# Kernel tuning notes

Measured on AMD Instinct MI355X. Metric: run time of the kernel, lower is better.

Reference implementation:

```python
import jax, jax.numpy as jnp
import numpy as np

HID = 1024
BATCH = 32
SRC = 2048

def setup_inputs() -> dict:
    key = jax.random.key(0)
    k1, k2, k3, k4, k5 = jax.random.split(key, 5)
    hidden = jax.random.normal(k1, (BATCH, HID), dtype=jnp.float32)
    encoder_outputs = jax.random.normal(k2, (BATCH, SRC, HID), dtype=jnp.float32)
    # nn.Linear(2H, H): weight [H, 2H], bias [H]
    lim = 1.0 / np.sqrt(2 * HID)
    attn_w = jax.random.uniform(k3, (HID, 2 * HID), dtype=jnp.float32, minval=-lim, maxval=lim)
    attn_b = jax.random.uniform(k4, (HID,), dtype=jnp.float32, minval=-lim, maxval=lim)
    v = jax.random.uniform(k5, (HID,), dtype=jnp.float32)  # torch.rand
    return {"hidden": hidden, "encoder_outputs": encoder_outputs,
            "attn_w": attn_w, "attn_b": attn_b, "v": v}

def reference(hidden, encoder_outputs, attn_w, attn_b, v):
    # Split the concat linear: cat([hidden, enc]) @ W^T == hidden @ Wh^T + enc @ We^T
    w_h = attn_w[:, :HID]          # [H, H] acts on repeated hidden
    w_e = attn_w[:, HID:]          # [H, H] acts on encoder outputs
    # energy: [B, S, H]
    energy = jnp.tanh(
        jnp.einsum('bh,oh->bo', hidden, w_h)[:, None, :]
        + jnp.einsum('bsh,oh->bso', encoder_outputs, w_e)
        + attn_b
    )
    scores = jnp.einsum('bso,o->bs', energy, v)  # [B, S]
    return jax.nn.softmax(scores, axis=1)
```

## Files before the change

### kernel.cpp

```cpp
#include <hip/hip_runtime.h>
#include <hip/hip_bf16.h>

#define HID   1024
#define NBATCH 32
#define SRC   2048
#define MROWS (NBATCH * SRC)

typedef _Float16 f16;
typedef f16  f16x8 __attribute__((ext_vector_type(8)));
typedef f16  f16x4 __attribute__((ext_vector_type(4)));
typedef float f32x4 __attribute__((ext_vector_type(4)));

__device__ __forceinline__ void gload_lds16(const void* g, void* l) {
  __builtin_amdgcn_global_load_lds(
      (const __attribute__((address_space(1))) void*)g,
      (__attribute__((address_space(3))) void*)l, 16, 0, 0);
}

__device__ __forceinline__ float fast_tanh(float x) {
  x = fminf(fmaxf(x, -15.f), 15.f);
  float e = __expf(2.f * x);
  return (e - 1.f) / (e + 1.f);
}

__global__ void convw_k(const float* __restrict__ attn_w, f16* __restrict__ Wf) {
  int idx = blockIdx.x * 256 + threadIdx.x;
  int j = idx * 4;
  int o = j >> 10, h = j & 1023;
  f32x4 d = *(const f32x4*)(attn_w + (size_t)o * 2048 + HID + h);
  f16x4 q = { (f16)d[0], (f16)d[1], (f16)d[2], (f16)d[3] };
  *(f16x4*)(Wf + (size_t)o * HID + h) = q;
}

__global__ void hvec_k(const float* __restrict__ hidden,
                       const float* __restrict__ attn_w,
                       const float* __restrict__ attn_b,
                       float* __restrict__ hvec) {
  int idx = blockIdx.x * 256 + threadIdx.x;
  int b = idx >> 10, o = idx & 1023;
  const float* wrow = attn_w + (size_t)o * 2048;
  const float* hrow = hidden + (size_t)b * HID;
  float acc = 0.f;
  for (int h = 0; h < HID; h += 4) {
    f32x4 wv = *(const f32x4*)(wrow + h);
    f32x4 hv = *(const f32x4*)(hrow + h);
    acc += wv[0]*hv[0] + wv[1]*hv[1] + wv[2]*hv[2] + wv[3]*hv[3];
  }
  hvec[idx] = acc + attn_b[o];
}

__global__ __launch_bounds__(256, 2) void gemm_fused(
    const float* __restrict__ A,
    const f16*  __restrict__ Wf,
    const float* __restrict__ hvec,
    const float* __restrict__ v,
    float* __restrict__ part)
{
  __shared__ __align__(16) f16 lA[128][32];
  __shared__ __align__(16) f16 lB[128][32];
  __shared__ float sc[128];

  int bid = blockIdx.x;
  int x = bid & 7;
  int j = bid >> 3;
  int m_idx = x * 64 + (j >> 3);
  int n_idx = j & 7;
  long row0 = (long)m_idx * 128;
  int  o0   = n_idx * 128;
  int  b    = (int)(row0 >> 11);

  int tid = threadIdx.x;
  int l = tid & 63, w = tid >> 6;
  int wr = w >> 1, wc = w & 1;
  int lr = l & 15, lg = l >> 4;

  f32x4 acc[4][4];
#pragma unroll
  for (int m = 0; m < 4; ++m)
#pragma unroll
    for (int n = 0; n < 4; ++n) acc[m][n] = (f32x4){0.f, 0.f, 0.f, 0.f};

  const float* Abase = A + row0 * 1024;

  for (int k0 = 0; k0 < 1024; k0 += 32) {
    __syncthreads();
#pragma unroll
    for (int i = 0; i < 2; ++i) {
      int rr = (i * 256 + tid) >> 2;
      const f16* src = Wf + (size_t)(o0 + rr) * HID + k0 + (tid & 3) * 8;
      char* ldsb = (char*)&lB[0][0] + i * 4096 + w * 1024;
      gload_lds16(src, ldsb);
    }
#pragma unroll
    for (int i = 0; i < 4; ++i) {
      int ja = i * 256 + tid;
      int arow = ja >> 3, ac4 = ja & 7;
      f32x4 d = *(const f32x4*)(Abase + (size_t)arow * 1024 + k0 + ac4 * 4);
      f16x4 q = { (f16)d[0], (f16)d[1], (f16)d[2], (f16)d[3] };
      *(f16x4*)&lA[arow][ac4 * 4] = q;
    }
    __syncthreads();
    f16x8 aF[4], bF[4];
#pragma unroll
    for (int m = 0; m < 4; ++m)
      aF[m] = *(const f16x8*)&lA[wr * 64 + m * 16 + lr][lg * 8];
#pragma unroll
    for (int n = 0; n < 4; ++n)
      bF[n] = *(const f16x8*)&lB[wc * 64 + n * 16 + lr][lg * 8];
#pragma unroll
    for (int m = 0; m < 4; ++m)
#pragma unroll
      for (int n = 0; n < 4; ++n)
        acc[m][n] = __builtin_amdgcn_mfma_f32_16x16x32_f16(aF[m], bF[n], acc[m][n], 0, 0, 0);
  }

  float hv[4], vv[4];
#pragma unroll
  for (int n = 0; n < 4; ++n) {
    int o = o0 + wc * 64 + n * 16 + lr;
    hv[n] = hvec[b * HID + o];
    vv[n] = v[o];
  }
  float myv[4][4];
#pragma unroll
  for (int m = 0; m < 4; ++m) {
#pragma unroll
    for (int r = 0; r < 4; ++r) {
      float s = 0.f;
#pragma unroll
      for (int n = 0; n < 4; ++n) {
        float e = fast_tanh(acc[m][n][r] + hv[n]);
        s += e * vv[n];
      }
      s += __shfl_xor(s, 1);
      s += __shfl_xor(s, 2);
      s += __shfl_xor(s, 4);
      s += __shfl_xor(s, 8);
      myv[m][r] = s;
    }
  }
  if (wc == 0 && lr == 0) {
#pragma unroll
    for (int m = 0; m < 4; ++m)
#pragma unroll
      for (int r = 0; r < 4; ++r)
        sc[wr * 64 + m * 16 + lg * 4 + r] = myv[m][r];
  }
  __syncthreads();
  if (wc == 1 && lr == 0) {
#pragma unroll
    for (int m = 0; m < 4; ++m)
#pragma unroll
      for (int r = 0; r < 4; ++r)
        sc[wr * 64 + m * 16 + lg * 4 + r] += myv[m][r];
  }
  __syncthreads();
  if (tid < 128)
    part[(size_t)n_idx * MROWS + row0 + tid] = sc[tid];
}

__global__ void softmax_k(const float* __restrict__ part, float* __restrict__ out) {
  int b = blockIdx.x;
  __shared__ float srow[SRC];
  __shared__ float red[8];
  int tid = threadIdx.x;

  float lmax = -1e30f;
  for (int i = tid; i < SRC; i += 256) {
    float s = 0.f;
#pragma unroll
    for (int t = 0; t < 8; ++t)
      s += part[(size_t)t * MROWS + (size_t)b * SRC + i];
    srow[i] = s;
    lmax = fmaxf(lmax, s);
  }
#pragma unroll
  for (int off = 32; off >= 1; off >>= 1)
    lmax = fmaxf(lmax, __shfl_xor(lmax, off));
  if ((tid & 63) == 0) red[tid >> 6] = lmax;
  __syncthreads();
  float bmax = fmaxf(fmaxf(red[0], red[1]), fmaxf(red[2], red[3]));

  float lsum = 0.f;
  for (int i = tid; i < SRC; i += 256) {
    float e = __expf(srow[i] - bmax);
    srow[i] = e;
    lsum += e;
  }
#pragma unroll
  for (int off = 32; off >= 1; off >>= 1)
    lsum += __shfl_xor(lsum, off);
  if ((tid & 63) == 0) red[4 + (tid >> 6)] = lsum;
  __syncthreads();
  float inv = 1.f / (red[4] + red[5] + red[6] + red[7]);
  for (int i = tid; i < SRC; i += 256)
    out[(size_t)b * SRC + i] = srow[i] * inv;
}

extern "C" void kernel_launch(void* const* d_in, const int* in_sizes, int n_in,
                              void* d_out, int out_size, void* d_ws, size_t ws_size,
                              hipStream_t stream) {
  const float* hidden = (const float*)d_in[0];
  const float* enc    = (const float*)d_in[1];
  const float* attn_w = (const float*)d_in[2];
  const float* attn_b = (const float*)d_in[3];
  const float* v      = (const float*)d_in[4];
  float* out = (float*)d_out;

  char* ws = (char*)d_ws;
  f16*   Wf   = (f16*)ws;
  float* hv   = (float*)(ws + (2u << 20));
  float* part = (float*)(ws + (2u << 20) + (512u << 10));

  convw_k<<<1024, 256, 0, stream>>>(attn_w, Wf);
  hvec_k <<<128,  256, 0, stream>>>(hidden, attn_w, attn_b, hv);
  gemm_fused<<<4096, 256, 0, stream>>>(enc, Wf, hv, v, part);
  softmax_k<<<NBATCH, 256, 0, stream>>>(part, out);
}
```

Baseline: 257.4 us.

## Double-buffer 256x256x64 GEMM tiles with swizzled LDS and staged loads

```diff
diff --git a/kernel.cpp b/kernel.cpp
--- a/kernel.cpp
+++ b/kernel.cpp
@@ -1,26 +1,34 @@
 #include <hip/hip_runtime.h>
 #include <hip/hip_bf16.h>
 
-#define HID   1024
+#define HID    1024
 #define NBATCH 32
-#define SRC   2048
-#define MROWS (NBATCH * SRC)
+#define SRC    2048
+#define MROWS  (NBATCH * SRC)
+#define BM     256
+#define BN     256
+#define BK     64
+#define NTILES (HID / BK)
 
 typedef _Float16 f16;
-typedef f16  f16x8 __attribute__((ext_vector_type(8)));
-typedef f16  f16x4 __attribute__((ext_vector_type(4)));
+typedef f16   f16x8 __attribute__((ext_vector_type(8)));
+typedef f16   f16x4 __attribute__((ext_vector_type(4)));
 typedef float f32x4 __attribute__((ext_vector_type(4)));
 
-__device__ __forceinline__ void gload_lds16(const void* g, void* l) {
-  __builtin_amdgcn_global_load_lds(
-      (const __attribute__((address_space(1))) void*)g,
-      (__attribute__((address_space(3))) void*)l, 16, 0, 0);
-}
+#define BAR()   asm volatile("s_barrier" ::: "memory")
+#define LGKM0() asm volatile("s_waitcnt lgkmcnt(0)" ::: "memory")
 
 __device__ __forceinline__ float fast_tanh(float x) {
   x = fminf(fmaxf(x, -15.f), 15.f);
   float e = __expf(2.f * x);
   return (e - 1.f) / (e + 1.f);
+}
+
+__device__ __forceinline__ f16* LAp(char* lds, int c, int row, int col) {
+  return (f16*)(lds + c * 65536 + row * 128 + ((col ^ ((row & 7) << 3)) << 1));
+}
+__device__ __forceinline__ f16* LBp(char* lds, int c, int row, int col) {
+  return (f16*)(lds + c * 65536 + 32768 + row * 128 + ((col ^ ((row & 7) << 3)) << 1));
 }
 
 __global__ void convw_k(const float* __restrict__ attn_w, f16* __restrict__ Wf) {
@@ -49,114 +57,127 @@
   hvec[idx] = acc + attn_b[o];
 }
 
-__global__ __launch_bounds__(256, 2) void gemm_fused(
+
+#define CVT8(lo, hi) (f16x8){ (f16)(lo)[0], (f16)(lo)[1], (f16)(lo)[2], (f16)(lo)[3], \
+                              (f16)(hi)[0], (f16)(hi)[1], (f16)(hi)[2], (f16)(hi)[3] }
+
+#define ISSUE_A1(t) { const float* p_ = Ab + (size_t)srow * HID + (t) * BK + scolh; \
+  sa0 = *(const f32x4*)p_; sa1 = *(const f32x4*)(p_ + 4); \
+  sa2 = *(const f32x4*)(p_ + 8); sa3 = *(const f32x4*)(p_ + 12); }
+#define ISSUE_A2(t) { const float* p_ = Ab + (size_t)srow * HID + (t) * BK + scolh + 16; \
+  sa4 = *(const f32x4*)p_; sa5 = *(const f32x4*)(p_ + 4); \
+  sa6 = *(const f32x4*)(p_ + 8); sa7 = *(const f32x4*)(p_ + 12); }
+#define ISSUE_B(t)  { const f16* p_ = Bb + (size_t)srow * HID + (t) * BK + scolh; \
+  sb0 = *(const f16x8*)p_; sb1 = *(const f16x8*)(p_ + 8); \
+  sb2 = *(const f16x8*)(p_ + 16); sb3 = *(const f16x8*)(p_ + 24); }
+#define WRITE_A1(cc) { *(f16x8*)LAp(lds, cc, srow, scolh)      = CVT8(sa0, sa1); \
+                       *(f16x8*)LAp(lds, cc, srow, scolh + 8)  = CVT8(sa2, sa3); }
+#define WRITE_A2(cc) { *(f16x8*)LAp(lds, cc, srow, scolh + 16) = CVT8(sa4, sa5); \
+                       *(f16x8*)LAp(lds, cc, srow, scolh + 24) = CVT8(sa6, sa7); }
+#define WRITE_B(cc)  { *(f16x8*)LBp(lds, cc, srow, scolh)      = sb0; \
+                       *(f16x8*)LBp(lds, cc, srow, scolh + 8)  = sb1; \
+                       *(f16x8*)LBp(lds, cc, srow, scolh + 16) = sb2; \
+                       *(f16x8*)LBp(lds, cc, srow, scolh + 24) = sb3; }
+
+#define TILE_BODY(cC, tn, DOSTAGE) { \
+  const int cn_ = (cC) ^ 1; \
+  f16x8 bF[4][2]; \
+  _Pragma("unroll") for (int n = 0; n < 4; ++n) \
+  _Pragma("unroll") for (int ks = 0; ks < 2; ++ks) \
+    bF[n][ks] = *(const f16x8*)LBp(lds, (cC), wc * 64 + n * 16 + lr, ks * 32 + lg * 8); \
+  _Pragma("unroll") for (int p = 0; p < 4; ++p) { \
+    f16x8 aF[2][2]; \
+    _Pragma("unroll") for (int i = 0; i < 2; ++i) \
+    _Pragma("unroll") for (int ks = 0; ks < 2; ++ks) \
+      aF[i][ks] = *(const f16x8*)LAp(lds, (cC), wr * 128 + (p * 2 + i) * 16 + lr, ks * 32 + lg * 8); \
+    if (DOSTAGE) { \
+      if (p == 0) { ISSUE_A1(tn); } \
+      if (p == 1) { ISSUE_A2(tn); ISSUE_B(tn); } \
+      if (p == 2) { WRITE_A1(cn_); } \
+      if (p == 3) { WRITE_A2(cn_); WRITE_B(cn_); } \
+    } \
+    __builtin_amdgcn_s_setprio(1); \
+    _Pragma("unroll") for (int ks = 0; ks < 2; ++ks) \
+    _Pragma("unroll") for (int i = 0; i < 2; ++i) \
+    _Pragma("unroll") for (int n = 0; n < 4; ++n) \
+      acc[p * 2 + i][n] = __builtin_amdgcn_mfma_f32_16x16x32_f16(aF[i][ks], bF[n][ks], acc[p * 2 + i][n], 0, 0, 0); \
+    __builtin_amdgcn_s_setprio(0); \
+    if (p == 3) { LGKM0(); } \
+    BAR(); \
+  } }
+
+__global__ __launch_bounds__(512, 2) void gemm_fused(
     const float* __restrict__ A,
     const f16*  __restrict__ Wf,
     const float* __restrict__ hvec,
     const float* __restrict__ v,
     float* __restrict__ part)
 {
-  __shared__ __align__(16) f16 lA[128][32];
-  __shared__ __align__(16) f16 lB[128][32];
-  __shared__ float sc[128];
+  extern __shared__ __align__(16) char lds[];
 
   int bid = blockIdx.x;
-  int x = bid & 7;
-  int j = bid >> 3;
-  int m_idx = x * 64 + (j >> 3);
-  int n_idx = j & 7;
-  long row0 = (long)m_idx * 128;
-  int  o0   = n_idx * 128;
-  int  b    = (int)(row0 >> 11);
+  int wg = (bid & 7) * 128 + (bid >> 3);
+  int m_idx = wg >> 2, n_idx = wg & 3;
+  long row0 = (long)m_idx * BM;
+  int o0 = n_idx * BN;
+  int b = (int)(row0 >> 11);
 
   int tid = threadIdx.x;
   int l = tid & 63, w = tid >> 6;
-  int wr = w >> 1, wc = w & 1;
+  int wr = w >> 2, wc = w & 3;
   int lr = l & 15, lg = l >> 4;
 
-  f32x4 acc[4][4];
-#pragma unroll
-  for (int m = 0; m < 4; ++m)
+  int srow = tid >> 1, scolh = (tid & 1) * 32;
+
+  const float* Ab = A + row0 * HID;
+  const f16*   Bb = Wf + (size_t)o0 * HID;
+
+  f32x4 acc[8][4];
+#pragma unroll
+  for (int m = 0; m < 8; ++m)
 #pragma unroll
     for (int n = 0; n < 4; ++n) acc[m][n] = (f32x4){0.f, 0.f, 0.f, 0.f};
 
-  const float* Abase = A + row0 * 1024;
-
-  for (int k0 = 0; k0 < 1024; k0 += 32) {
-    __syncthreads();
-#pragma unroll
-    for (int i = 0; i < 2; ++i) {
-      int rr = (i * 256 + tid) >> 2;
-      const f16* src = Wf + (size_t)(o0 + rr) * HID + k0 + (tid & 3) * 8;
-      char* ldsb = (char*)&lB[0][0] + i * 4096 + w * 1024;
-      gload_lds16(src, ldsb);
-    }
-#pragma unroll
-    for (int i = 0; i < 4; ++i) {
-      int ja = i * 256 + tid;
-      int arow = ja >> 3, ac4 = ja & 7;
-      f32x4 d = *(const f32x4*)(Abase + (size_t)arow * 1024 + k0 + ac4 * 4);
-      f16x4 q = { (f16)d[0], (f16)d[1], (f16)d[2], (f16)d[3] };
-      *(f16x4*)&lA[arow][ac4 * 4] = q;
-    }
-    __syncthreads();
-    f16x8 aF[4], bF[4];
-#pragma unroll
-    for (int m = 0; m < 4; ++m)
-      aF[m] = *(const f16x8*)&lA[wr * 64 + m * 16 + lr][lg * 8];
-#pragma unroll
-    for (int n = 0; n < 4; ++n)
-      bF[n] = *(const f16x8*)&lB[wc * 64 + n * 16 + lr][lg * 8];
-#pragma unroll
-    for (int m = 0; m < 4; ++m)
-#pragma unroll
-      for (int n = 0; n < 4; ++n)
-        acc[m][n] = __builtin_amdgcn_mfma_f32_16x16x32_f16(aF[m], bF[n], acc[m][n], 0, 0, 0);
-  }
-
-  float hv[4], vv[4];
+  f32x4 sa0, sa1, sa2, sa3, sa4, sa5, sa6, sa7;
+  f16x8 sb0, sb1, sb2, sb3;
+
+  ISSUE_A1(0); ISSUE_A2(0); ISSUE_B(0);
+  WRITE_A1(0); WRITE_A2(0); WRITE_B(0);
+  LGKM0(); BAR();
+
+  for (int T = 0; T < NTILES - 1; ++T) {
+    const int c = T & 1;
+    TILE_BODY(c, T + 1, 1);
+  }
+  TILE_BODY((NTILES - 1) & 1, 0, 0);
+
+  float hvv[4], vvv[4];
 #pragma unroll
   for (int n = 0; n < 4; ++n) {
     int o = o0 + wc * 64 + n * 16 + lr;
-    hv[n] = hvec[b * HID + o];
-    vv[n] = v[o];
-  }
-  float myv[4][4];
-#pragma unroll
-  for (int m = 0; m < 4; ++m) {
+    hvv[n] = hvec[b * HID + o];
+    vvv[n] = v[o];
+  }
+  float* scf = (float*)lds;
+  __syncthreads();
+#pragma unroll
+  for (int m = 0; m < 8; ++m) {
 #pragma unroll
     for (int r = 0; r < 4; ++r) {
       float s = 0.f;
 #pragma unroll
-      for (int n = 0; n < 4; ++n) {
-        float e = fast_tanh(acc[m][n][r] + hv[n]);
-        s += e * vv[n];
-      }
-      s += __shfl_xor(s, 1);
-      s += __shfl_xor(s, 2);
-      s += __shfl_xor(s, 4);
-      s += __shfl_xor(s, 8);
-      myv[m][r] = s;
+      for (int n = 0; n < 4; ++n)
+        s += fast_tanh(acc[m][n][r] + hvv[n]) * vvv[n];
+      s += __shfl_xor(s, 1); s += __shfl_xor(s, 2);
+      s += __shfl_xor(s, 4); s += __shfl_xor(s, 8);
+      if (lr == 0) scf[wc * 256 + wr * 128 + m * 16 + lg * 4 + r] = s;
     }
   }
-  if (wc == 0 && lr == 0) {
-#pragma unroll
-    for (int m = 0; m < 4; ++m)
-#pragma unroll
-      for (int r = 0; r < 4; ++r)
-        sc[wr * 64 + m * 16 + lg * 4 + r] = myv[m][r];
-  }
-  __syncthreads();
-  if (wc == 1 && lr == 0) {
-#pragma unroll
-    for (int m = 0; m < 4; ++m)
-#pragma unroll
-      for (int r = 0; r < 4; ++r)
-        sc[wr * 64 + m * 16 + lg * 4 + r] += myv[m][r];
-  }
-  __syncthreads();
-  if (tid < 128)
-    part[(size_t)n_idx * MROWS + row0 + tid] = sc[tid];
+  __syncthreads();
+  if (tid < 256) {
+    float sum = scf[tid] + scf[256 + tid] + scf[512 + tid] + scf[768 + tid];
+    part[(size_t)n_idx * MROWS + row0 + tid] = sum;
+  }
 }
 
 __global__ void softmax_k(const float* __restrict__ part, float* __restrict__ out) {
@@ -169,7 +190,7 @@
   for (int i = tid; i < SRC; i += 256) {
     float s = 0.f;
 #pragma unroll
-    for (int t = 0; t < 8; ++t)
+    for (int t = 0; t < 4; ++t)
       s += part[(size_t)t * MROWS + (size_t)b * SRC + i];
     srow[i] = s;
     lmax = fmaxf(lmax, s);
@@ -214,6 +235,6 @@
 
   convw_k<<<1024, 256, 0, stream>>>(attn_w, Wf);
   hvec_k <<<128,  256, 0, stream>>>(hidden, attn_w, attn_b, hv);
-  gemm_fused<<<4096, 256, 0, stream>>>(enc, Wf, hv, v, part);
+  gemm_fused<<<1024, 512, 131072, stream>>>(enc, Wf, hv, v, part);
   softmax_k<<<NBATCH, 256, 0, stream>>>(part, out);
 }
```

Result: slower. 319.6 us (+24.2%).

## Pre-convert encoder outputs to f16 and use a pipelined swizzled MFMA GEMM

Applied to the files above, without the earlier changes.

```diff
diff --git a/kernel.cpp b/kernel.cpp
--- a/kernel.cpp
+++ b/kernel.cpp
@@ -1,15 +1,18 @@
 #include <hip/hip_runtime.h>
 #include <hip/hip_bf16.h>
 
-#define HID   1024
+#define HID    1024
 #define NBATCH 32
-#define SRC   2048
-#define MROWS (NBATCH * SRC)
+#define SRC    2048
+#define MROWS  (NBATCH * SRC)
 
 typedef _Float16 f16;
-typedef f16  f16x8 __attribute__((ext_vector_type(8)));
-typedef f16  f16x4 __attribute__((ext_vector_type(4)));
+typedef f16   f16x8 __attribute__((ext_vector_type(8)));
+typedef f16   f16x4 __attribute__((ext_vector_type(4)));
 typedef float f32x4 __attribute__((ext_vector_type(4)));
+
+#define BAR()    asm volatile("s_barrier" ::: "memory")
+#define VMCNT(n) asm volatile("s_waitcnt vmcnt(" #n ")" ::: "memory")
 
 __device__ __forceinline__ void gload_lds16(const void* g, void* l) {
   __builtin_amdgcn_global_load_lds(
@@ -49,25 +52,133 @@
   hvec[idx] = acc + attn_b[o];
 }
 
-__global__ __launch_bounds__(256, 2) void gemm_fused(
-    const float* __restrict__ A,
+__global__ void convA_k(const float* __restrict__ A, f16* __restrict__ Af) {
+  size_t i = ((size_t)blockIdx.x * 256 + threadIdx.x) * 8;
+  f32x4 d0 = *(const f32x4*)(A + i);
+  f32x4 d1 = *(const f32x4*)(A + i + 4);
+  f16x8 q = { (f16)d0[0], (f16)d0[1], (f16)d0[2], (f16)d0[3],
+              (f16)d1[0], (f16)d1[1], (f16)d1[2], (f16)d1[3] };
+  *(f16x8*)(Af + i) = q;
+}
+
+
+#define STG(T) do { \
+  char* la_ = lds + ((T) % 3) * 49152; char* lb_ = la_ + 32768; \
+  _Pragma("unroll") for (int i_ = 0; i_ < 4; ++i_) \
+    gload_lds16(Ab + (size_t)(i_ * 64 + w * 8 + sr8) * HID + (T) * 64 + scol, \
+                la_ + i_ * 8192 + w * 1024); \
+  _Pragma("unroll") for (int i_ = 0; i_ < 2; ++i_) \
+    gload_lds16(Bb + (size_t)(i_ * 64 + w * 8 + sr8) * HID + (T) * 64 + scol, \
+                lb_ + i_ * 8192 + w * 1024); } while (0)
+
+__global__ __launch_bounds__(512, 2) void gemm_f16(
+    const f16*  __restrict__ Af,
     const f16*  __restrict__ Wf,
     const float* __restrict__ hvec,
     const float* __restrict__ v,
     float* __restrict__ part)
 {
+  extern __shared__ __align__(16) char lds[];
+
+  int bid = blockIdx.x;
+  int wg = (bid & 7) * 256 + (bid >> 3);
+  int m_idx = wg >> 3, n_idx = wg & 7;
+  long row0 = (long)m_idx * 256;
+  int o0 = n_idx * 128;
+  int b = (int)(row0 >> 11);
+
+  int tid = threadIdx.x;
+  int l = tid & 63, w = tid >> 6;
+  int wr = w >> 2, wc = w & 3;
+  int lr = l & 15, lg = l >> 4;
+  int sr8 = l >> 3;
+  int scol = ((l & 7) ^ sr8) << 3;
+  int sw = (lr & 7) << 3;
+
+  const f16* Ab = Af + row0 * HID;
+  const f16* Bb = Wf + (size_t)o0 * HID;
+
+  f32x4 acc[8][2];
+#pragma unroll
+  for (int m = 0; m < 8; ++m) {
+    acc[m][0] = (f32x4){0.f, 0.f, 0.f, 0.f};
+    acc[m][1] = (f32x4){0.f, 0.f, 0.f, 0.f};
+  }
+
+  STG(0); STG(1);
+  VMCNT(6); BAR();
+
+  for (int T = 0; T < 16; ++T) {
+    if (T + 2 < 16) STG(T + 2);
+    const char* la = lds + (T % 3) * 49152;
+    const char* lb = la + 32768;
+
+    f16x8 bF[2][2];
+#pragma unroll
+    for (int n = 0; n < 2; ++n)
+#pragma unroll
+      for (int ks = 0; ks < 2; ++ks)
+        bF[n][ks] = *(const f16x8*)(lb + (wc * 32 + n * 16 + lr) * 128 +
+                                    (((ks * 32 + lg * 8) ^ sw) << 1));
+    __builtin_amdgcn_s_setprio(1);
+#pragma unroll
+    for (int m = 0; m < 8; ++m) {
+      const char* ra = la + (wr * 128 + m * 16 + lr) * 128;
+      f16x8 a0 = *(const f16x8*)(ra + (((lg * 8) ^ sw) << 1));
+      f16x8 a1 = *(const f16x8*)(ra + (((32 + lg * 8) ^ sw) << 1));
+      acc[m][0] = __builtin_amdgcn_mfma_f32_16x16x32_f16(a0, bF[0][0], acc[m][0], 0, 0, 0);
+      acc[m][1] = __builtin_amdgcn_mfma_f32_16x16x32_f16(a0, bF[1][0], acc[m][1], 0, 0, 0);
+      acc[m][0] = __builtin_amdgcn_mfma_f32_16x16x32_f16(a1, bF[0][1], acc[m][0], 0, 0, 0);
+      acc[m][1] = __builtin_amdgcn_mfma_f32_16x16x32_f16(a1, bF[1][1], acc[m][1], 0, 0, 0);
+    }
+    __builtin_amdgcn_s_setprio(0);
+
+    if (T < 14)       { VMCNT(6); BAR(); }
+    else if (T == 14) { VMCNT(0); BAR(); }
+  }
+
+  float hvv[2], vvv[2];
+#pragma unroll
+  for (int n = 0; n < 2; ++n) {
+    int o = o0 + wc * 32 + n * 16 + lr;
+    hvv[n] = hvec[b * HID + o];
+    vvv[n] = v[o];
+  }
+  float* scf = (float*)lds;
+  __syncthreads();
+#pragma unroll
+  for (int m = 0; m < 8; ++m) {
+#pragma unroll
+    for (int r = 0; r < 4; ++r) {
+      float s = fast_tanh(acc[m][0][r] + hvv[0]) * vvv[0]
+              + fast_tanh(acc[m][1][r] + hvv[1]) * vvv[1];
+      s += __shfl_xor(s, 1); s += __shfl_xor(s, 2);
+      s += __shfl_xor(s, 4); s += __shfl_xor(s, 8);
+      if (lr == 0) scf[wc * 256 + wr * 128 + m * 16 + lg * 4 + r] = s;
+    }
+  }
+  __syncthreads();
+  if (tid < 256)
+    part[(size_t)n_idx * MROWS + row0 + tid] =
+        scf[tid] + scf[256 + tid] + scf[512 + tid] + scf[768 + tid];
+}
+
+__global__ __launch_bounds__(256, 2) void gemm_fb(
+    const float* __restrict__ A, const f16* __restrict__ Wf,
+    const float* __restrict__ hvec, const float* __restrict__ v,
+    float* __restrict__ part)
+{
   __shared__ __align__(16) f16 lA[128][32];
   __shared__ __align__(16) f16 lB[128][32];
   __shared__ float sc[128];
 
   int bid = blockIdx.x;
-  int x = bid & 7;
-  int j = bid >> 3;
+  int x = bid & 7, j = bid >> 3;
   int m_idx = x * 64 + (j >> 3);
   int n_idx = j & 7;
   long row0 = (long)m_idx * 128;
-  int  o0   = n_idx * 128;
-  int  b    = (int)(row0 >> 11);
+  int o0 = n_idx * 128;
+  int b = (int)(row0 >> 11);
 
   int tid = threadIdx.x;
   int l = tid & 63, w = tid >> 6;
@@ -128,14 +239,10 @@
     for (int r = 0; r < 4; ++r) {
       float s = 0.f;
 #pragma unroll
-      for (int n = 0; n < 4; ++n) {
-        float e = fast_tanh(acc[m][n][r] + hv[n]);
-        s += e * vv[n];
-      }
-      s += __shfl_xor(s, 1);
-      s += __shfl_xor(s, 2);
-      s += __shfl_xor(s, 4);
-      s += __shfl_xor(s, 8);
+      for (int n = 0; n < 4; ++n)
+        s += fast_tanh(acc[m][n][r] + hv[n]) * vv[n];
+      s += __shfl_xor(s, 1); s += __shfl_xor(s, 2);
+      s += __shfl_xor(s, 4); s += __shfl_xor(s, 8);
       myv[m][r] = s;
     }
   }
@@ -209,11 +316,20 @@
 
   char* ws = (char*)d_ws;
   f16*   Wf   = (f16*)ws;
-  float* hv   = (float*)(ws + (2u << 20));
-  float* part = (float*)(ws + (2u << 20) + (512u << 10));
+  float* hv   = (float*)(ws + (2ull << 20));
+  float* part = (float*)(ws + (2ull << 20) + (128ull << 10));
+  f16*   Af   = (f16*)(ws + (8ull << 20));
+
+  const size_t WS_NEEDED = (8ull << 20) + (128ull << 20) + (1ull << 20);
 
   convw_k<<<1024, 256, 0, stream>>>(attn_w, Wf);
   hvec_k <<<128,  256, 0, stream>>>(hidden, attn_w, attn_b, hv);
-  gemm_fused<<<4096, 256, 0, stream>>>(enc, Wf, hv, v, part);
+
+  if (ws_size >= WS_NEEDED) {
+    convA_k<<<32768, 256, 0, stream>>>(enc, Af);
+    gemm_f16<<<2048, 512, 147456, stream>>>(Af, Wf, hv, v, part);
+  } else {
+    gemm_fb<<<4096, 256, 0, stream>>>(enc, Wf, hv, v, part);
+  }
   softmax_k<<<NBATCH, 256, 0, stream>>>(part, out);
 }
```

Measured after the change: 310.7 us. 20.7% more time.
